# Kernel tuning notes

Hardware: AMD Instinct MI355X
Metric: run time of the kernel (lower is better)

Reference implementation:

```python
import jax, jax.numpy as jnp
import numpy as np

NUM_STUFF = 53
NUM_THING = 80
NUM_CLASSES = NUM_STUFF + NUM_THING  # 133
OBJ_THR = 0.4
OVERLAP_THR = 0.8
B, Q, HM, WM = 2, 100, 160, 160  # mask res = image/4


def setup_inputs() -> dict:
    key = jax.random.key(0)
    k1, k2 = jax.random.split(key)
    # Scale logits so some queries exceed the 0.4 softmax-score threshold.
    logits = 5.0 * jax.random.normal(k1, (B, Q, NUM_CLASSES + 1), dtype=jnp.float32)
    # Give each query a dominant blob (10x10 tile grid) so the greedy
    # overlap-threshold fusion accepts a realistic set of segments.
    th, tw = HM // 10, WM // 10
    tile_id = (jnp.arange(HM) // th)[:, None] * 10 + (jnp.arange(WM) // tw)[None, :]  # [HM,WM]
    bias = jnp.where(tile_id[None, :, :] == jnp.arange(Q)[:, None, None], 8.0, -8.0)  # [Q,HM,WM]
    noise = jax.random.normal(k2, (B, Q, HM, WM), dtype=jnp.float32)
    masks = noise + bias[None]
    return {"logits": logits, "masks": masks, "H": 640, "W": 640}


def reference(logits, masks, H, W):
    """Vectorized, jit-compatible port of Mask2FormerPanoptic._panoptic_merge.

    logits: [B, Q, C+1], masks: [B, Q, h, w]. Returns (sem_seg [B,C,H,W] f32,
    panoptic_seg [B,H,W] int32). The sequential greedy loop is equivalent to a
    per-query acceptance test (areas are loop-invariant) + cumsum id assignment,
    because argmax assigns each pixel to exactly one query.
    """
    Qn = masks.shape[1]

    def merge(lg, mk):
        probs = jax.nn.softmax(lg, axis=-1)               # [Q, C+1]
        scores = jnp.max(probs, axis=-1)                  # [Q]
        labels = jnp.argmax(probs, axis=-1)               # [Q]
        keep = (labels < NUM_CLASSES) & (scores > OBJ_THR)
        # sigmoid then bilinear upsample (half-pixel centers == align_corners=False)
        up = jax.image.resize(jax.nn.sigmoid(mk), (Qn, H, W), method='bilinear')  # [Q,H,W]
        prob_masks = jnp.where(keep[:, None, None], scores[:, None, None] * up, -1.0)
        mask_ids = jnp.argmax(prob_masks, axis=0)         # [H,W]
        mask_area = jnp.zeros((Qn,), jnp.int32).at[mask_ids.ravel()].add(1)  # [Q]
        orig_area = jnp.sum(up >= 0.5, axis=(1, 2))       # [Q]
        accepted = keep & (mask_area > 0) & (orig_area > 0) & (
            mask_area.astype(jnp.float32) > OVERLAP_THR * orig_area.astype(jnp.float32))
        ids = jnp.cumsum(accepted.astype(jnp.int32))      # greedy 1-based segment ids
        panoptic = jnp.where(accepted[mask_ids], ids[mask_ids], 0).astype(jnp.int32)
        masked = jnp.where(accepted[:, None, None], up, 0.0)
        # sem_seg[cls] = max over accepted queries with that class (zeros init)
        sem = jnp.zeros((NUM_CLASSES, H, W), jnp.float32).at[labels].max(masked)
        return sem, panoptic

    return jax.vmap(merge)(logits, masks)
```

## Files before the change

### kernel.cpp

```cpp
#include <hip/hip_runtime.h>
#include <stdint.h>
#include <math.h>

#define NB   2
#define NQ   100
#define NCLS 133
#define NCL1 134
#define HM   160
#define WM   160
#define HO   640
#define WO   640
#define G    8
#define NCELL (HM*WM)
#define SEMROWS 16

typedef float f32x4 __attribute__((ext_vector_type(4)));

static __device__ __forceinline__ int clampi(int v, int lo, int hi){ return v<lo?lo:(v>hi?hi:v); }
static __device__ __forceinline__ double dsig(float x){ return 1.0/(1.0+exp(-(double)x)); }

__global__ void k_classify(const float* __restrict__ logits, double* __restrict__ scores,
                           int* __restrict__ labels, int* __restrict__ keepf,
                           int* __restrict__ kq, int* __restrict__ Kc,
                           int* __restrict__ marea, int* __restrict__ oarea)
{
  int t = threadIdx.x;
  for (int i=t;i<NB*NQ;i+=blockDim.x){ marea[i]=0; oarea[i]=0; }
  if (t < NB*NQ){
    const float* l = logits + (size_t)t*NCL1;
    float mx = l[0]; int am = 0;
    for (int c=1;c<NCL1;++c){ float v=l[c]; if (v>mx){ mx=v; am=c; } }
    double s = 0.0;
    for (int c=0;c<NCL1;++c) s += exp((double)l[c] - (double)mx);
    double sc = 1.0/s;
    scores[t] = sc; labels[t] = am;
    keepf[t] = (am < NCLS && sc > 0.4) ? 1 : 0;
  }
  __syncthreads();
  if (t < NB){
    int k = 0;
    for (int q=0;q<NQ;++q) if (keepf[t*NQ+q]) kq[t*NQ + (k++)] = q;
    Kc[t] = k;
  }
}

__global__ void k_sigmoid(const float* __restrict__ masks, double* __restrict__ sig64,
                          float* __restrict__ sig32, const int* __restrict__ keepf)
{
  int gid = blockIdx.x*blockDim.x + threadIdx.x;
  int bq  = gid / (HM*WM/4);
  if (!keepf[bq]) return;
  float4 v = reinterpret_cast<const float4*>(masks)[gid];
  double o0 = dsig(v.x), o1 = dsig(v.y), o2 = dsig(v.z), o3 = dsig(v.w);
  double2 d0; d0.x=o0; d0.y=o1;
  double2 d1; d1.x=o2; d1.y=o3;
  reinterpret_cast<double2*>(sig64)[gid*2]   = d0;
  reinterpret_cast<double2*>(sig64)[gid*2+1] = d1;
  float4 f; f.x=(float)o0; f.y=(float)o1; f.z=(float)o2; f.w=(float)o3;
  reinterpret_cast<float4*>(sig32)[gid] = f;
}

__global__ __launch_bounds__(256) void k_argmax_part(const double* __restrict__ sig64,
        const double* __restrict__ scores, const int* __restrict__ kq,
        const int* __restrict__ Kc, unsigned long long* __restrict__ ppack,
        int* __restrict__ oarea)
{
  __shared__ double patch[18][18];
  __shared__ int oacc[16];
  const int b    = blockIdx.z / G;
  const int g    = blockIdx.z % G;
  const int tid  = threadIdx.x;
  const int tx   = tid & 15, ty = tid >> 4;
  const int cj   = blockIdx.x*16 + tx;
  const int ci   = blockIdx.y*16 + ty;
  const int gr0  = blockIdx.y*16 - 1;
  const int gc0  = blockIdx.x*16 - 1;
  const int K   = Kc[b];
  const int Kg  = (K + G - 1) / G;
  const int k0  = g*Kg;
  const int k1  = min(K, k0 + Kg);

  if (tid < 16) oacc[tid] = 0;

  double best[4][4];
  int    bq[4][4];
  #pragma unroll
  for (int r=0;r<4;++r)
    #pragma unroll
    for (int s=0;s<4;++s){ best[r][s] = -1.0; bq[r][s] = 0; }

  const int i0 = tid,     p0r = i0/18, p0c = i0-18*p0r;
  const int i1 = tid+256; int p1r = i1/18, p1c = i1-18*p1r;
  const int a0 = clampi(gr0+p0r,0,HM-1)*WM + clampi(gc0+p0c,0,WM-1);
  const int a1 = clampi(gr0+p1r,0,HM-1)*WM + clampi(gc0+p1c,0,WM-1);

  __syncthreads();

  for (int k=k0;k<k1;++k){
    const int    q  = kq[b*NQ+k];
    const double sc = scores[b*NQ+q];
    const double* sp = sig64 + (size_t)(b*NQ + q)*HM*WM;

    patch[p0r][p0c] = sp[a0];
    if (i1 < 324) patch[p1r][p1c] = sp[a1];
    __syncthreads();

    double v[3][3];
    #pragma unroll
    for (int rr=0;rr<3;++rr)
      #pragma unroll
      for (int cc=0;cc<3;++cc)
        v[rr][cc] = patch[ty+rr][tx+cc];

    int cnt = 0;
    #pragma unroll
    for (int r=0;r<4;++r){
      const double wa = (r==0)?0.375:(r==1)?0.125:(r==2)?0.875:0.625;
      const double wb = (r==0)?0.625:(r==1)?0.875:(r==2)?0.125:0.375;
      const int ra = (r<2)?0:1, rb = ra+1;
      const bool vedge = (r<2) ? (ci==0) : (ci==HM-1);
      const int  vsel  = (r<2) ? rb : ra;
      double t0 = vedge ? v[vsel][0] : (wa*v[ra][0] + wb*v[rb][0]);
      double t1 = vedge ? v[vsel][1] : (wa*v[ra][1] + wb*v[rb][1]);
      double t2 = vedge ? v[vsel][2] : (wa*v[ra][2] + wb*v[rb][2]);
      double u[4];
      u[0] = (cj==0)    ? t1 : (0.375*t0 + 0.625*t1);
      u[1] = (cj==0)    ? t1 : (0.125*t0 + 0.875*t1);
      u[2] = (cj==WM-1) ? t1 : (0.875*t1 + 0.125*t2);
      u[3] = (cj==WM-1) ? t1 : (0.625*t1 + 0.375*t2);
      #pragma unroll
      for (int s=0;s<4;++s){
        cnt += (u[s] >= 0.5) ? 1 : 0;
        double val = sc*u[s];
        if (val > best[r][s]){ best[r][s] = val; bq[r][s] = q; }
      }
    }
    #pragma unroll
    for (int o2=32;o2>0;o2>>=1) cnt += __shfl_down(cnt, o2);
    if ((tid & 63) == 0) atomicAdd(&oacc[k-k0], cnt);

    __syncthreads();
  }

  if (tid < k1-k0){
    int cv = oacc[tid];
    if (cv) atomicAdd(&oarea[b*NQ + kq[b*NQ+k0+tid]], cv);
  }

  const int cell = ci*WM + cj;
  #pragma unroll
  for (int r=0;r<4;++r)
    #pragma unroll
    for (int s=0;s<4;++s){
      unsigned long long pk = 0ULL;
      if (k0 < k1)
        pk = ((unsigned long long)__double_as_longlong(best[r][s]) & ~127ULL)
           | (unsigned long long)(127 - bq[r][s]);
      size_t idx = ((size_t)((b*G + g)*16 + r*4 + s))*NCELL + cell;
      ppack[idx] = pk;
    }
}

static __device__ __forceinline__ int decode_q(unsigned long long v){
  int q = 127 - (int)(v & 127ULL);
  return clampi(q, 0, NQ-1);
}

__global__ __launch_bounds__(256) void k_argmax_comb(const unsigned long long* __restrict__ ppack,
        uint32_t* __restrict__ mids, int* __restrict__ marea)
{
  __shared__ int hist[NQ];
  const int b   = blockIdx.z;
  const int tid = threadIdx.x;
  const int tx  = tid & 15, ty = tid >> 4;
  const int cj  = blockIdx.x*16 + tx;
  const int ci  = blockIdx.y*16 + ty;
  const int cell= ci*WM + cj;

  for (int i=tid;i<NQ;i+=256) hist[i]=0;
  __syncthreads();

  int bqa[16];
  #pragma unroll
  for (int rs=0;rs<16;++rs){
    unsigned long long cur = 0ULL;
    #pragma unroll
    for (int g2=0;g2<G;++g2){
      unsigned long long v = ppack[((size_t)((b*G + g2)*16 + rs))*NCELL + cell];
      if (v > cur) cur = v;
    }
    bqa[rs] = decode_q(cur);
  }

  #pragma unroll
  for (int r=0;r<4;++r){
    uint32_t w = (uint32_t)bqa[r*4+0] | ((uint32_t)bqa[r*4+1]<<8)
               | ((uint32_t)bqa[r*4+2]<<16) | ((uint32_t)bqa[r*4+3]<<24);
    int y = 4*ci + r;
    mids[(b*HO + y)*(WO/4) + cj] = w;
  }
  #pragma unroll
  for (int rs=0;rs<16;++rs)
    atomicAdd(&hist[bqa[rs]], 1);
  __syncthreads();
  for (int i=tid;i<NQ;i+=256)
    if (hist[i]) atomicAdd(&marea[b*NQ+i], hist[i]);
}

__global__ void k_finalize(const int* __restrict__ keepf, const int* __restrict__ labels,
                           const int* __restrict__ marea, const int* __restrict__ oarea,
                           float* __restrict__ fid, int* __restrict__ chanoff,
                           int* __restrict__ sortedq)
{
  const int b = blockIdx.x;
  const int tid = threadIdx.x;
  __shared__ int acc[NQ], lab[NQ], cntS[NCLS], start[NCLS];
  if (tid < NQ){
    int i = b*NQ + tid;
    int ma = marea[i], oa = oarea[i];
    acc[tid] = (keepf[i] && ma>0 && oa>0 && ((double)ma > 0.8*(double)oa)) ? 1 : 0;
    lab[tid] = labels[i];
  }
  if (tid < NCLS) cntS[tid]=0;
  __syncthreads();
  if (tid == 0){
    int A = 0;
    for (int q=0;q<NQ;++q){
      if (acc[q]){ A++; fid[b*NQ+q] = (float)A; cntS[lab[q]]++; }
      else fid[b*NQ+q] = 0.0f;
    }
    int off = 0;
    for (int c=0;c<NCLS;++c){ start[c]=off; chanoff[b*NCL1+c]=off; off += cntS[c]; }
    chanoff[b*NCL1+NCLS] = off;
    for (int q=0;q<NQ;++q)
      if (acc[q]){ int c=lab[q]; sortedq[b*NQ + start[c]] = q; start[c]++; }
  }
}

__global__ void k_pan(const uint32_t* __restrict__ mids, const float* __restrict__ fid,
                      float* __restrict__ out)
{
  int t = blockIdx.x*blockDim.x + threadIdx.x;
  int b = t / (HO*WO/4);
  uint32_t w = mids[t];
  f32x4 o;
  o.x = fid[b*NQ + (w & 255u)];
  o.y = fid[b*NQ + ((w>>8) & 255u)];
  o.z = fid[b*NQ + ((w>>16) & 255u)];
  o.w = fid[b*NQ + (w>>24)];
  __builtin_nontemporal_store(o,
      reinterpret_cast<f32x4*>(out) + (size_t)NB*NCLS*(HO*(size_t)WO/4) + t);
}

__global__ __launch_bounds__(256) void k_sem(const float* __restrict__ sig32,
        const int* __restrict__ chanoff, const int* __restrict__ sortedq,
        float* __restrict__ out)
{
  const int bc = blockIdx.y;
  const int b  = bc / NCLS, c = bc - b*NCLS;
  const int y0 = blockIdx.x * SEMROWS;
  const int ci0 = y0 >> 2;
  const int tid = threadIdx.x;
  const int s0 = chanoff[b*NCL1+c], s1 = chanoff[b*NCL1+c+1];

  __shared__ float row[6][WM];

  f32x4 acc[10];
  #pragma unroll
  for (int ch=0;ch<10;++ch) acc[ch] = (f32x4)(0.f);

  for (int i=s0;i<s1;++i){
    const int q = sortedq[b*NQ+i];
    const float* sp = sig32 + (size_t)(b*NQ+q)*HM*WM;
    for (int i2=tid;i2<6*WM;i2+=256){
      int jr = i2/WM, jc = i2 - jr*WM;
      int gi = clampi(ci0 + jr - 1, 0, HM-1);
      row[jr][jc] = sp[gi*WM + jc];
    }
    __syncthreads();
    #pragma unroll
    for (int ch=0;ch<10;++ch){
      const int idx = ch*256 + tid;
      const int yo  = idx / WM;
      const int x4  = idx - yo*WM;
      const int y   = y0 + yo;
      const int ci  = y >> 2, r = y & 3;
      const int ciL = ci - ci0 + 1;
      const int ra  = (r<2) ? ciL-1 : ciL;
      const int rb  = ra + 1;
      const bool vedge = (r<2) ? (ci==0) : (ci==HM-1);
      const int cm = max(x4-1,0), cp = min(x4+1,WM-1);
      const float wa = (r==0)?0.375f:(r==1)?0.125f:(r==2)?0.875f:0.625f;
      const float wb = (r==0)?0.625f:(r==1)?0.875f:(r==2)?0.125f:0.375f;
      float am=row[ra][cm], a0=row[ra][x4], ap=row[ra][cp];
      float bm=row[rb][cm], b0=row[rb][x4], bp=row[rb][cp];
      float t0 = vedge ? ((r<2) ? bm : am) : (wa*am + wb*bm);
      float t1 = vedge ? ((r<2) ? b0 : a0) : (wa*a0 + wb*b0);
      float t2 = vedge ? ((r<2) ? bp : ap) : (wa*ap + wb*bp);
      float u0 = (x4==0)    ? t1 : (0.375f*t0 + 0.625f*t1);
      float u1 = (x4==0)    ? t1 : (0.125f*t0 + 0.875f*t1);
      float u2 = (x4==WM-1) ? t1 : (0.875f*t1 + 0.125f*t2);
      float u3 = (x4==WM-1) ? t1 : (0.625f*t1 + 0.375f*t2);
      acc[ch].x = fmaxf(acc[ch].x, u0);
      acc[ch].y = fmaxf(acc[ch].y, u1);
      acc[ch].z = fmaxf(acc[ch].z, u2);
      acc[ch].w = fmaxf(acc[ch].w, u3);
    }
    __syncthreads();
  }

  f32x4* ob = reinterpret_cast<f32x4*>(out) + ((size_t)bc*HO + y0)*(WO/4);
  #pragma unroll
  for (int ch=0;ch<10;++ch)
    __builtin_nontemporal_store(acc[ch], ob + ch*256 + tid);
}

extern "C" void kernel_launch(void* const* d_in, const int* in_sizes, int n_in,
                              void* d_out, int out_size, void* d_ws, size_t ws_size,
                              hipStream_t stream)
{
  const float* logits = (const float*)d_in[0];
  const float* masks  = (const float*)d_in[1];
  float* out = (float*)d_out;

  char* ws = (char*)d_ws;
  size_t off = 0;
  auto alloc = [&](size_t bytes)->void*{
    void* p = ws + off; off = (off + bytes + 255) & ~(size_t)255; return p;
  };
  double*   sig64   = (double*)  alloc((size_t)NB*NQ*HM*WM*sizeof(double));
  float*    sig32   = (float*)   alloc((size_t)NB*NQ*HM*WM*sizeof(float));
  unsigned long long* ppack = (unsigned long long*)
                               alloc((size_t)NB*G*16*NCELL*sizeof(unsigned long long));
  uint32_t* mids    = (uint32_t*)alloc((size_t)NB*HO*(WO/4)*sizeof(uint32_t));
  double*   scores  = (double*)  alloc(NB*NQ*sizeof(double));
  int*      labels  = (int*)     alloc(NB*NQ*sizeof(int));
  int*      keepf   = (int*)     alloc(NB*NQ*sizeof(int));
  int*      kq      = (int*)     alloc(NB*NQ*sizeof(int));
  int*      Kc      = (int*)     alloc(NB*sizeof(int));
  int*      marea   = (int*)     alloc(NB*NQ*sizeof(int));
  int*      oarea   = (int*)     alloc(NB*NQ*sizeof(int));
  float*    fid     = (float*)   alloc(NB*NQ*sizeof(float));
  int*      chanoff = (int*)     alloc(NB*NCL1*sizeof(int));
  int*      sortedq = (int*)     alloc(NB*NQ*sizeof(int));

  hipLaunchKernelGGL(k_classify, dim3(1), dim3(256), 0, stream,
                     logits, scores, labels, keepf, kq, Kc, marea, oarea);
  hipLaunchKernelGGL(k_sigmoid, dim3((NB*NQ*HM*WM/4)/256), dim3(256), 0, stream,
                     masks, sig64, sig32, keepf);
  hipLaunchKernelGGL(k_argmax_part, dim3(WM/16, HM/16, NB*G), dim3(256), 0, stream,
                     sig64, scores, kq, Kc, ppack, oarea);
  hipLaunchKernelGGL(k_argmax_comb, dim3(WM/16, HM/16, NB), dim3(256), 0, stream,
                     ppack, mids, marea);
  hipLaunchKernelGGL(k_finalize, dim3(NB), dim3(192), 0, stream,
                     keepf, labels, marea, oarea, fid, chanoff, sortedq);
  hipLaunchKernelGGL(k_pan, dim3((NB*HO*WO/4)/256), dim3(256), 0, stream,
                     mids, fid, out);
  hipLaunchKernelGGL(k_sem, dim3(HO/SEMROWS, NB*NCLS), dim3(256), 0, stream,
                     sig32, chanoff, sortedq, out);
}
```

Before: 226.3 us.

## Fuse classify with sigmoid and panoptic with semantic kernels, double sem rows

Merges the classify and sigmoid launches into one grid, where the extra last block does classification. Because that block runs concurrently, sigmoid no longer skips non-kept queries and computes all of them. Merges the panoptic id write into the semantic kernel as extra grid rows and doubles SEMROWS to 32, so each block covers more output and reuses its staged rows. The aims are fewer launches and less overhead, at the cost of extra sigmoid work and higher register pressure from 20 accumulators.

```diff
diff --git a/kernel.cpp b/kernel.cpp
--- a/kernel.cpp
+++ b/kernel.cpp
@@ -12,18 +12,32 @@
 #define WO   640
 #define G    8
 #define NCELL (HM*WM)
-#define SEMROWS 16
+#define SEMROWS 32
+#define SIGBLKS ((NB*NQ*HM*WM/4)/256)
 
 typedef float f32x4 __attribute__((ext_vector_type(4)));
 
 static __device__ __forceinline__ int clampi(int v, int lo, int hi){ return v<lo?lo:(v>hi?hi:v); }
 static __device__ __forceinline__ double dsig(float x){ return 1.0/(1.0+exp(-(double)x)); }
 
-__global__ void k_classify(const float* __restrict__ logits, double* __restrict__ scores,
-                           int* __restrict__ labels, int* __restrict__ keepf,
-                           int* __restrict__ kq, int* __restrict__ Kc,
-                           int* __restrict__ marea, int* __restrict__ oarea)
-{
+__global__ void k_sig_cls(const float* __restrict__ masks, double* __restrict__ sig64,
+                          float* __restrict__ sig32, const float* __restrict__ logits,
+                          double* __restrict__ scores, int* __restrict__ labels,
+                          int* __restrict__ keepf, int* __restrict__ kq, int* __restrict__ Kc,
+                          int* __restrict__ marea, int* __restrict__ oarea)
+{
+  if (blockIdx.x < SIGBLKS){
+    int gid = blockIdx.x*blockDim.x + threadIdx.x;
+    float4 v = reinterpret_cast<const float4*>(masks)[gid];
+    double o0 = dsig(v.x), o1 = dsig(v.y), o2 = dsig(v.z), o3 = dsig(v.w);
+    double2 d0; d0.x=o0; d0.y=o1;
+    double2 d1; d1.x=o2; d1.y=o3;
+    reinterpret_cast<double2*>(sig64)[gid*2]   = d0;
+    reinterpret_cast<double2*>(sig64)[gid*2+1] = d1;
+    float4 f; f.x=(float)o0; f.y=(float)o1; f.z=(float)o2; f.w=(float)o3;
+    reinterpret_cast<float4*>(sig32)[gid] = f;
+    return;
+  }
   int t = threadIdx.x;
   for (int i=t;i<NB*NQ;i+=blockDim.x){ marea[i]=0; oarea[i]=0; }
   if (t < NB*NQ){
@@ -42,22 +56,6 @@
     for (int q=0;q<NQ;++q) if (keepf[t*NQ+q]) kq[t*NQ + (k++)] = q;
     Kc[t] = k;
   }
-}
-
-__global__ void k_sigmoid(const float* __restrict__ masks, double* __restrict__ sig64,
-                          float* __restrict__ sig32, const int* __restrict__ keepf)
-{
-  int gid = blockIdx.x*blockDim.x + threadIdx.x;
-  int bq  = gid / (HM*WM/4);
-  if (!keepf[bq]) return;
-  float4 v = reinterpret_cast<const float4*>(masks)[gid];
-  double o0 = dsig(v.x), o1 = dsig(v.y), o2 = dsig(v.z), o3 = dsig(v.w);
-  double2 d0; d0.x=o0; d0.y=o1;
-  double2 d1; d1.x=o2; d1.y=o3;
-  reinterpret_cast<double2*>(sig64)[gid*2]   = d0;
-  reinterpret_cast<double2*>(sig64)[gid*2+1] = d1;
-  float4 f; f.x=(float)o0; f.y=(float)o1; f.z=(float)o2; f.w=(float)o3;
-  reinterpret_cast<float4*>(sig32)[gid] = f;
 }
 
 __global__ __launch_bounds__(256) void k_argmax_part(const double* __restrict__ sig64,
@@ -237,49 +235,53 @@
   }
 }
 
-__global__ void k_pan(const uint32_t* __restrict__ mids, const float* __restrict__ fid,
-                      float* __restrict__ out)
-{
-  int t = blockIdx.x*blockDim.x + threadIdx.x;
-  int b = t / (HO*WO/4);
-  uint32_t w = mids[t];
-  f32x4 o;
-  o.x = fid[b*NQ + (w & 255u)];
-  o.y = fid[b*NQ + ((w>>8) & 255u)];
-  o.z = fid[b*NQ + ((w>>16) & 255u)];
-  o.w = fid[b*NQ + (w>>24)];
-  __builtin_nontemporal_store(o,
-      reinterpret_cast<f32x4*>(out) + (size_t)NB*NCLS*(HO*(size_t)WO/4) + t);
-}
-
-__global__ __launch_bounds__(256) void k_sem(const float* __restrict__ sig32,
+__global__ __launch_bounds__(256) void k_sem_pan(const float* __restrict__ sig32,
         const int* __restrict__ chanoff, const int* __restrict__ sortedq,
+        const uint32_t* __restrict__ mids, const float* __restrict__ fid,
         float* __restrict__ out)
 {
+  const int tid = threadIdx.x;
+  if (blockIdx.y >= NB*NCLS){
+    const int blk = (blockIdx.y - NB*NCLS)*gridDim.x + blockIdx.x;
+    f32x4* ob = reinterpret_cast<f32x4*>(out) + (size_t)NB*NCLS*(HO*(size_t)WO/4);
+    #pragma unroll
+    for (int j=0;j<20;++j){
+      int t = (blk*20 + j)*256 + tid;
+      int b = t / (HO*WO/4);
+      uint32_t w = mids[t];
+      f32x4 o;
+      o.x = fid[b*NQ + (w & 255u)];
+      o.y = fid[b*NQ + ((w>>8) & 255u)];
+      o.z = fid[b*NQ + ((w>>16) & 255u)];
+      o.w = fid[b*NQ + (w>>24)];
+      __builtin_nontemporal_store(o, ob + t);
+    }
+    return;
+  }
+
   const int bc = blockIdx.y;
   const int b  = bc / NCLS, c = bc - b*NCLS;
   const int y0 = blockIdx.x * SEMROWS;
   const int ci0 = y0 >> 2;
-  const int tid = threadIdx.x;
   const int s0 = chanoff[b*NCL1+c], s1 = chanoff[b*NCL1+c+1];
 
-  __shared__ float row[6][WM];
-
-  f32x4 acc[10];
-  #pragma unroll
-  for (int ch=0;ch<10;++ch) acc[ch] = (f32x4)(0.f);
+  __shared__ float row[10][WM];
+
+  f32x4 acc[20];
+  #pragma unroll
+  for (int ch=0;ch<20;++ch) acc[ch] = (f32x4)(0.f);
 
   for (int i=s0;i<s1;++i){
     const int q = sortedq[b*NQ+i];
     const float* sp = sig32 + (size_t)(b*NQ+q)*HM*WM;
-    for (int i2=tid;i2<6*WM;i2+=256){
+    for (int i2=tid;i2<10*WM;i2+=256){
       int jr = i2/WM, jc = i2 - jr*WM;
       int gi = clampi(ci0 + jr - 1, 0, HM-1);
       row[jr][jc] = sp[gi*WM + jc];
     }
     __syncthreads();
     #pragma unroll
-    for (int ch=0;ch<10;++ch){
+    for (int ch=0;ch<20;++ch){
       const int idx = ch*256 + tid;
       const int yo  = idx / WM;
       const int x4  = idx - yo*WM;
@@ -311,7 +313,7 @@
 
   f32x4* ob = reinterpret_cast<f32x4*>(out) + ((size_t)bc*HO + y0)*(WO/4);
   #pragma unroll
-  for (int ch=0;ch<10;++ch)
+  for (int ch=0;ch<20;++ch)
     __builtin_nontemporal_store(acc[ch], ob + ch*256 + tid);
 }
 
@@ -344,18 +346,15 @@
   int*      chanoff = (int*)     alloc(NB*NCL1*sizeof(int));
   int*      sortedq = (int*)     alloc(NB*NQ*sizeof(int));
 
-  hipLaunchKernelGGL(k_classify, dim3(1), dim3(256), 0, stream,
-                     logits, scores, labels, keepf, kq, Kc, marea, oarea);
-  hipLaunchKernelGGL(k_sigmoid, dim3((NB*NQ*HM*WM/4)/256), dim3(256), 0, stream,
-                     masks, sig64, sig32, keepf);
+  hipLaunchKernelGGL(k_sig_cls, dim3(SIGBLKS+1), dim3(256), 0, stream,
+                     masks, sig64, sig32, logits, scores, labels, keepf, kq, Kc,
+                     marea, oarea);
   hipLaunchKernelGGL(k_argmax_part, dim3(WM/16, HM/16, NB*G), dim3(256), 0, stream,
                      sig64, scores, kq, Kc, ppack, oarea);
   hipLaunchKernelGGL(k_argmax_comb, dim3(WM/16, HM/16, NB), dim3(256), 0, stream,
                      ppack, mids, marea);
   hipLaunchKernelGGL(k_finalize, dim3(NB), dim3(192), 0, stream,
                      keepf, labels, marea, oarea, fid, chanoff, sortedq);
-  hipLaunchKernelGGL(k_pan, dim3((NB*HO*WO/4)/256), dim3(256), 0, stream,
-                     mids, fid, out);
-  hipLaunchKernelGGL(k_sem, dim3(HO/SEMROWS, NB*NCLS), dim3(256), 0, stream,
-                     sig32, chanoff, sortedq, out);
-}
+  hipLaunchKernelGGL(k_sem_pan, dim3(HO/SEMROWS, NB*NCLS+2), dim3(256), 0, stream,
+                     sig32, chanoff, sortedq, mids, fid, out);
+}
```

Measured after the change: 217.6 us (median of 2 runs). -3.9%, faster.
